# Optimization experiments

Hardware: AMD Instinct MI355X
Metric: run time of the kernel (lower is better)

The kernel has to match this reference:

```python
import jax, jax.numpy as jnp
import numpy as np

B, L, H = 16, 2048, 768
INNER = max(H // 2, 32)
RADIUS = 2
K_STEPS = 4
ETA = 0.1
ETA_DECAY = 0.9
MU_MAX = 10.0
LAM = 0.1


def _window_edges(length, radius):
    ei, ej = [], []
    for r in range(1, radius + 1):
        i = np.arange(length - r)
        ei.append(i)
        ej.append(i + r)
    return (jnp.asarray(np.concatenate(ei), jnp.int32),
            jnp.asarray(np.concatenate(ej), jnp.int32))


def setup_inputs() -> dict:
    key = jax.random.key(0)
    ks = jax.random.split(key, 6)
    hidden = jax.random.normal(ks[0], (B, L, H), jnp.float32)
    attention_mask = jnp.ones((B, L), jnp.int32)  # uniform full lengths -> single bucket, window path
    w1 = jax.random.normal(ks[1], (2, INNER), jnp.float32) * 0.2
    b1 = jnp.zeros((INNER,), jnp.float32)
    w2 = jax.random.normal(ks[2], (INNER, 1), jnp.float32) * 0.05
    b2 = jnp.zeros((1,), jnp.float32)
    wq = jax.random.normal(ks[3], (H, H), jnp.float32) * (1.0 / np.sqrt(H))
    bq = jnp.zeros((H,), jnp.float32)
    gamma = jnp.ones((H,), jnp.float32)
    beta = jnp.zeros((H,), jnp.float32)
    edges_i, edges_j = _window_edges(L, RADIUS)
    return dict(hidden=hidden, attention_mask=attention_mask, w1=w1, b1=b1,
                w2=w2, b2=b2, wq=wq, bq=bq, gamma=gamma, beta=beta,
                edges_i=edges_i, edges_j=edges_j)


def _friction(hidden, w1, b1, w2, b2, wq, bq, gamma, beta, edges_i, edges_j):
    eps = 1e-6
    q = hidden @ wq + bq                      # [B,L,H]
    state = hidden
    mu = None
    for step in range(K_STEPS):
        # edge weights from current state (recompute_mu=True)
        h_i = state[:, edges_i]               # [B,E,H] gather
        h_j = state[:, edges_j]
        diff = h_i - h_j
        dist = jnp.sqrt(jnp.sum(diff * diff, -1))
        n_i = jnp.maximum(jnp.sqrt(jnp.sum(h_i * h_i, -1)), eps)
        n_j = jnp.maximum(jnp.sqrt(jnp.sum(h_j * h_j, -1)), eps)
        cos = jnp.sum(h_i * h_j, -1) / (n_i * n_j)
        feats = jnp.stack([dist, cos], -1)    # [B,E,2]
        mid = jax.nn.gelu(feats @ w1 + b1, approximate=False)
        mu = jnp.minimum(jax.nn.softplus((mid @ w2 + b2)[..., 0]) + 1e-5, MU_MAX)  # [B,E]
        # normalized weighted graph Laplacian applied to state
        w = mu[..., None] * diff
        deg = jnp.zeros((state.shape[0], state.shape[1]), state.dtype)
        deg = deg.at[:, edges_i].add(mu).at[:, edges_j].add(mu)
        inv = jnp.maximum(deg, 1e-6) ** -0.5
        w = w * (inv[:, edges_i] * inv[:, edges_j])[..., None]
        lap = jnp.zeros_like(state).at[:, edges_i].add(w).at[:, edges_j].add(-w)
        state = state - (ETA * ETA_DECAY ** step) * (lap - q)
        # 1D chain smoothing with replicated boundaries
        left = jnp.concatenate([state[:, :1], state[:, :-1]], 1)
        right = jnp.concatenate([state[:, 1:], state[:, -1:]], 1)
        state = state - LAM * (2 * state - left - right)
    # edge energy with last mu and final state: 0.5 * sum_e mu_e ||s_i - s_j||^2
    df = state[:, edges_i] - state[:, edges_j]
    energy = 0.5 * jnp.sum(mu * jnp.sum(df * df, -1), axis=1)  # [B]
    res = state + hidden
    mean = jnp.mean(res, -1, keepdims=True)
    var = jnp.mean((res - mean) ** 2, -1, keepdims=True)
    out = (res - mean) / jnp.sqrt(var + 1e-5) * gamma + beta
    return out, energy


def reference(hidden, attention_mask, w1, b1, w2, b2, wq, bq, gamma, beta, edges_i, edges_j):
    # all masks are full-length ones -> single bucket, batched window path
    return _friction(hidden, w1, b1, w2, b2, wq, bq, gamma, beta, edges_i, edges_j)
```

## Files before the change

### kernel.cpp

```cpp
#include <hip/hip_runtime.h>
#include <hip/hip_bf16.h>
#include <math.h>

#define B_ 16
#define L_ 2048
#define H_ 768
#define INNER_ 384
#define MU_MAX_ 10.0f
#define LAM_ 0.1f
#define EDGES_ (2 * L_ - 3)

typedef short v8bf __attribute__((ext_vector_type(8)));
typedef float v4f  __attribute__((ext_vector_type(4)));

static __device__ __forceinline__ float wave_sum(float v) {
    #pragma unroll
    for (int o = 32; o > 0; o >>= 1) v += __shfl_xor(v, o, 64);
    return v;
}

static __device__ __forceinline__ float dot4(const float4& a, const float4& b) {
    return a.x * b.x + a.y * b.y + a.z * b.z + a.w * b.w;
}

static __device__ __forceinline__ void fma4(float4& a, float c, float4 x) {
    a.x = fmaf(c, x.x, a.x); a.y = fmaf(c, x.y, a.y);
    a.z = fmaf(c, x.z, a.z); a.w = fmaf(c, x.w, a.w);
}

static __device__ __forceinline__ ushort f2bf(float x) {
    unsigned u = __float_as_uint(x);
    u += 0x7fffu + ((u >> 16) & 1u);
    return (ushort)(u >> 16);
}

__global__ __launch_bounds__(256) void conv_wqt_kernel(
    const float* __restrict__ wq, ushort* __restrict__ wt)
{
    __shared__ float tile[64][65];
    int k0 = blockIdx.x * 64, n0 = blockIdx.y * 64;
    int t = threadIdx.x;
    #pragma unroll
    for (int it = 0; it < 16; ++it) {
        int lin = t + it * 256;
        int r = lin >> 6, c = lin & 63;
        tile[r][c] = wq[(size_t)(k0 + r) * H_ + n0 + c];
    }
    __syncthreads();
    #pragma unroll
    for (int it = 0; it < 16; ++it) {
        int lin = t + it * 256;
        int r = lin >> 6, c = lin & 63;
        wt[(size_t)(n0 + r) * H_ + k0 + c] = f2bf(tile[c][r]);
    }
}

#define GBM 128
#define GBN 128
#define GBK 64
#define LSTR 72

__global__ __launch_bounds__(256) void gemm_q_kernel(
    const float* __restrict__ A32, const ushort* __restrict__ Wt,
    const float* __restrict__ bias, float* __restrict__ C)
{
    __shared__ ushort As[GBM * LSTR];
    __shared__ ushort Bs[GBN * LSTR];
    const int K = H_, N = H_;
    int idx = blockIdx.x;
    int c = idx & 7, rest = idx >> 3;
    int n0 = (rest % 6) * GBN;
    int m0 = ((rest / 6) * 8 + c) * GBM;
    int t = threadIdx.x;
    int lane = t & 63, w = t >> 6;
    int wm = (w & 1) * 64, wn = (w >> 1) * 64;
    int row16 = lane & 15, quad = lane >> 4;

    v4f acc[4][4];
    #pragma unroll
    for (int i = 0; i < 4; ++i)
        #pragma unroll
        for (int j = 0; j < 4; ++j)
            acc[i][j] = (v4f){0.f, 0.f, 0.f, 0.f};

    float4 pf0[4], pf1[4];
    v8bf pfB[4];
    #pragma unroll
    for (int it = 0; it < 4; ++it) {
        int lin = t + it * 256;
        int r = lin >> 3, s = lin & 7;
        const float* ap = A32 + (size_t)(m0 + r) * K + s * 8;
        pf0[it] = *(const float4*)ap;
        pf1[it] = *(const float4*)(ap + 4);
        pfB[it] = *(const v8bf*)(Wt + (size_t)(n0 + r) * K + s * 8);
    }

    for (int kt = 0; kt < 12; ++kt) {
        int k0 = kt * GBK;
        #pragma unroll
        for (int it = 0; it < 4; ++it) {
            int lin = t + it * 256;
            int r = lin >> 3, s = lin & 7;
            ushort tmp[8] = { f2bf(pf0[it].x), f2bf(pf0[it].y), f2bf(pf0[it].z), f2bf(pf0[it].w),
                              f2bf(pf1[it].x), f2bf(pf1[it].y), f2bf(pf1[it].z), f2bf(pf1[it].w) };
            *(v8bf*)&As[r * LSTR + s * 8] = *(v8bf*)tmp;
            *(v8bf*)&Bs[r * LSTR + s * 8] = pfB[it];
        }
        if (kt < 11) {
            int kn = k0 + GBK;
            #pragma unroll
            for (int it = 0; it < 4; ++it) {
                int lin = t + it * 256;
                int r = lin >> 3, s = lin & 7;
                const float* ap = A32 + (size_t)(m0 + r) * K + kn + s * 8;
                pf0[it] = *(const float4*)ap;
                pf1[it] = *(const float4*)(ap + 4);
                pfB[it] = *(const v8bf*)(Wt + (size_t)(n0 + r) * K + kn + s * 8);
            }
        }
        __syncthreads();
        #pragma unroll
        for (int h = 0; h < 2; ++h) {
            v8bf af[4], bfv[4];
            #pragma unroll
            for (int i = 0; i < 4; ++i)
                af[i] = *(v8bf*)&As[(wm + i * 16 + row16) * LSTR + h * 32 + quad * 8];
            #pragma unroll
            for (int j = 0; j < 4; ++j)
                bfv[j] = *(v8bf*)&Bs[(wn + j * 16 + row16) * LSTR + h * 32 + quad * 8];
            #pragma unroll
            for (int i = 0; i < 4; ++i)
                #pragma unroll
                for (int j = 0; j < 4; ++j)
                    acc[i][j] = __builtin_amdgcn_mfma_f32_16x16x32_bf16(
                        af[i], bfv[j], acc[i][j], 0, 0, 0);
        }
        __syncthreads();
    }
    #pragma unroll
    for (int j = 0; j < 4; ++j) {
        int ncol = n0 + wn + j * 16 + row16;
        float bqv = bias[ncol];
        #pragma unroll
        for (int i = 0; i < 4; ++i) {
            int mrow = m0 + wm + i * 16 + quad * 4;
            #pragma unroll
            for (int r = 0; r < 4; ++r)
                C[(size_t)(mrow + r) * N + ncol] = acc[i][j][r] + bqv;
        }
    }
}

__global__ __launch_bounds__(256) void mu_pair_kernel(
    const float* __restrict__ src,
    const float* __restrict__ w1, const float* __restrict__ b1,
    const float* __restrict__ w2, const float* __restrict__ b2,
    float* __restrict__ mu)
{
    int blk = blockIdx.x;
    int chunk = (blk & 7) * ((B_ * L_ / 8) / 8) + (blk >> 3);
    int b = chunk >> 8;
    int p0 = (chunk & 255) * 8;
    int w = threadIdx.x >> 6, lane = threadIdx.x & 63;
    int t0 = p0 + 2 * w;

    const float* sB = src + (size_t)b * L_ * H_;
    int r2 = min(t0 + 2, L_ - 1), r3 = min(t0 + 3, L_ - 1);
    const float4* x0p = (const float4*)(sB + (size_t)t0 * H_);
    const float4* x1p = (const float4*)(sB + (size_t)(t0 + 1) * H_);
    const float4* x2p = (const float4*)(sB + (size_t)r2 * H_);
    const float4* x3p = (const float4*)(sB + (size_t)r3 * H_);

    float ss0 = 0.f, ss1 = 0.f, ss2 = 0.f, ss3 = 0.f;
    float d1a = 0.f, d1b = 0.f, d2a = 0.f, d2b = 0.f;
    #pragma unroll
    for (int ch = 0; ch < 3; ++ch) {
        int off = ch * 64 + lane;
        float4 x0 = x0p[off], x1 = x1p[off], x2 = x2p[off], x3 = x3p[off];
        ss0 += dot4(x0, x0); ss1 += dot4(x1, x1);
        ss2 += dot4(x2, x2); ss3 += dot4(x3, x3);
        d1a += dot4(x0, x1); d1b += dot4(x1, x2);
        d2a += dot4(x0, x2); d2b += dot4(x1, x3);
    }
    ss0 = wave_sum(ss0); ss1 = wave_sum(ss1); ss2 = wave_sum(ss2); ss3 = wave_sum(ss3);
    d1a = wave_sum(d1a); d1b = wave_sum(d1b); d2a = wave_sum(d2a); d2b = wave_sum(d2b);

    float dist[4], cosv[4];
    {
        float si[4] = {ss0, ss0, ss1, ss1};
        float sj[4] = {ss1, ss2, ss2, ss3};
        float dd[4] = {d1a, d2a, d1b, d2b};
        #pragma unroll
        for (int e = 0; e < 4; ++e) {
            dist[e] = sqrtf(fmaxf(si[e] + sj[e] - 2.f * dd[e], 0.f));
            cosv[e] = dd[e] / (fmaxf(sqrtf(si[e]), 1e-6f) * fmaxf(sqrtf(sj[e]), 1e-6f));
        }
    }
    float acc[4] = {0.f, 0.f, 0.f, 0.f};
    #pragma unroll
    for (int k = 0; k < 6; ++k) {
        int u = k * 64 + lane;
        float wd = w1[u], wc = w1[INNER_ + u], bb = b1[u], wv = w2[u];
        #pragma unroll
        for (int e = 0; e < 4; ++e) {
            float z = fmaf(dist[e], wd, fmaf(cosv[e], wc, bb));
            float g = 0.5f * z * (1.f + erff(z * 0.70710678118654752f));
            acc[e] = fmaf(g, wv, acc[e]);
        }
    }
    #pragma unroll
    for (int e = 0; e < 4; ++e) acc[e] = wave_sum(acc[e]);

    float b2v = b2[0];
    float muv[4];
    #pragma unroll
    for (int e = 0; e < 4; ++e) {
        float a = acc[e] + b2v;
        float sp = fmaxf(a, 0.f) + log1pf(expf(-fabsf(a)));
        muv[e] = fminf(sp + 1e-5f, MU_MAX_);
    }
    if (lane == 0) {
        float* mB = mu + (size_t)b * EDGES_;
        mB[t0] = muv[0];
        if (t0 < L_ - 2) {
            mB[(L_ - 1) + t0] = muv[1];
            mB[t0 + 1] = muv[2];
            if (t0 + 1 < L_ - 2) mB[(L_ - 1) + t0 + 1] = muv[3];
        }
    }
}

template <int LN>
__global__ __launch_bounds__(256) void upd_quad_kernel(
    const float* __restrict__ src, const float* __restrict__ q,
    const float* __restrict__ mu, float* __restrict__ dst,
    const float* __restrict__ hidden, const float* __restrict__ gamma,
    const float* __restrict__ beta, float* __restrict__ lnout, float coef)
{
    int blk = blockIdx.x;
    int chunk = (blk & 7) * ((B_ * L_ / 16) / 8) + (blk >> 3);
    int b = chunk >> 7;
    int p0 = (chunk & 127) * 16;
    int w = threadIdx.x >> 6, lane = threadIdx.x & 63;
    int t0 = p0 + 4 * w;

    const float* mp = mu + (size_t)b * EDGES_;
    float M1[11], M2[12];
    #pragma unroll
    for (int j = 0; j < 11; ++j) {
        int u = t0 - 4 + j;
        M1[j] = (u >= 0 && u < L_ - 1) ? mp[u] : 0.f;
    }
    #pragma unroll
    for (int j = 0; j < 12; ++j) {
        int u = t0 - 5 + j;
        M2[j] = (u >= 0 && u < L_ - 2) ? mp[(L_ - 1) + u] : 0.f;
    }
    float IV[10];
    #pragma unroll
    for (int d = 0; d < 10; ++d) {
        int u = t0 - 3 + d;
        if (u < 0 || u >= L_) { IV[d] = 0.f; }
        else {
            float deg = M1[d + 1] + M1[d] + M2[d + 2] + M2[d];
            IV[d] = 1.f / sqrtf(fmaxf(deg, 1e-6f));
        }
    }
    float C[4][7], e[4][3];
    #pragma unroll
    for (int r = 0; r < 4; ++r) {
        int p = t0 + r;
        float gwv[3];
        gwv[0] = (p == 0) ? 0.f : LAM_;
        gwv[2] = (p == L_ - 1) ? 0.f : LAM_;
        gwv[1] = 1.f - 2.f * LAM_ + ((p == 0 || p == L_ - 1) ? LAM_ : 0.f);
        #pragma unroll
        for (int d = 0; d < 7; ++d) C[r][d] = 0.f;
        #pragma unroll
        for (int i = 0; i < 3; ++i) {
            int j = r + i;
            float g = gwv[i];
            float wm2 = M2[j + 2] * IV[j + 2] * IV[j];
            float wm1 = M1[j + 2] * IV[j + 2] * IV[j + 1];
            float wp1 = M1[j + 3] * IV[j + 2] * IV[j + 3];
            float wp2 = M2[j + 4] * IV[j + 2] * IV[j + 4];
            float wsum = wm2 + wm1 + wp1 + wp2;
            C[r][i]     = fmaf(g * coef, wm2, C[r][i]);
            C[r][i + 1] = fmaf(g * coef, wm1, C[r][i + 1]);
            C[r][i + 2] = fmaf(g, fmaf(-coef, wsum, 1.f), C[r][i + 2]);
            C[r][i + 3] = fmaf(g * coef, wp1, C[r][i + 3]);
            C[r][i + 4] = fmaf(g * coef, wp2, C[r][i + 4]);
            e[r][i] = g * coef;
        }
    }

    const float* sB = src + (size_t)b * L_ * H_;
    const float* qB = q + (size_t)b * L_ * H_;
    const float* sp[10];
    #pragma unroll
    for (int u = 0; u < 10; ++u)
        sp[u] = sB + (size_t)min(max(t0 - 3 + u, 0), L_ - 1) * H_;
    const float* qp[6];
    #pragma unroll
    for (int u = 0; u < 6; ++u)
        qp[u] = qB + (size_t)min(max(t0 - 1 + u, 0), L_ - 1) * H_;

    float* dA = dst + ((size_t)b * L_ + t0) * H_;
    float4 res[4][3];
    #pragma unroll
    for (int ch = 0; ch < 3; ++ch) {
        int off = ch * 64 + lane;
        float4 S[10], Q[6];
        #pragma unroll
        for (int u = 0; u < 10; ++u) S[u] = ((const float4*)sp[u])[off];
        #pragma unroll
        for (int u = 0; u < 6; ++u) Q[u] = ((const float4*)qp[u])[off];
        #pragma unroll
        for (int r = 0; r < 4; ++r) {
            float4 a = {0.f, 0.f, 0.f, 0.f};
            #pragma unroll
            for (int d = 0; d < 7; ++d) fma4(a, C[r][d], S[r + d]);
            #pragma unroll
            for (int i = 0; i < 3; ++i) fma4(a, e[r][i], Q[r + i]);
            ((float4*)(dA + (size_t)r * H_))[off] = a;
            if (LN) res[r][ch] = a;
        }
    }

    if (LN) {
        const float* hB = hidden + ((size_t)b * L_ + t0) * H_;
        float* oB = lnout + ((size_t)b * L_ + t0) * H_;
        float sum[4], sq[4];
        #pragma unroll
        for (int r = 0; r < 4; ++r) {
            sum[r] = 0.f; sq[r] = 0.f;
            #pragma unroll
            for (int ch = 0; ch < 3; ++ch) {
                int off = ch * 64 + lane;
                float4 h = ((const float4*)(hB + (size_t)r * H_))[off];
                float4 x = res[r][ch];
                x.x += h.x; x.y += h.y; x.z += h.z; x.w += h.w;
                res[r][ch] = x;
                sum[r] += x.x + x.y + x.z + x.w;
                sq[r]  += x.x * x.x + x.y * x.y + x.z * x.z + x.w * x.w;
            }
        }
        #pragma unroll
        for (int r = 0; r < 4; ++r) { sum[r] = wave_sum(sum[r]); sq[r] = wave_sum(sq[r]); }
        #pragma unroll
        for (int r = 0; r < 4; ++r) {
            float mean = sum[r] * (1.f / H_);
            float var  = sq[r] * (1.f / H_) - mean * mean;
            float rs = 1.f / sqrtf(var + 1e-5f);
            #pragma unroll
            for (int ch = 0; ch < 3; ++ch) {
                int off = ch * 64 + lane;
                float4 g4 = ((const float4*)gamma)[off];
                float4 b4 = ((const float4*)beta)[off];
                float4 x = res[r][ch];
                float4 o;
                o.x = (x.x - mean) * rs * g4.x + b4.x;
                o.y = (x.y - mean) * rs * g4.y + b4.y;
                o.z = (x.z - mean) * rs * g4.z + b4.z;
                o.w = (x.w - mean) * rs * g4.w + b4.w;
                ((float4*)(oB + (size_t)r * H_))[off] = o;
            }
        }
    }
}

__global__ void zero_energy_kernel(float* __restrict__ e) {
    if (threadIdx.x < B_) e[threadIdx.x] = 0.f;
}

#define EPW 16
__global__ __launch_bounds__(256) void energy_kernel(
    const float* __restrict__ state, const int* __restrict__ ei, const int* __restrict__ ej,
    const float* __restrict__ mu, float* __restrict__ energy, int E)
{
    __shared__ float red[4];
    int wib = threadIdx.x >> 6;
    int lane = threadIdx.x & 63;
    int nchunk = (E + 63) / 64;
    int b = blockIdx.x / nchunk;
    int chunk = blockIdx.x - b * nchunk;
    int e0 = chunk * 64 + wib * EPW;
    const float* base = state + (size_t)b * L_ * H_;
    const float* muB = mu + (size_t)b * E;
    float part = 0.f;
    for (int k = 0; k < EPW; ++k) {
        int e = e0 + k;
        if (e >= E) break;
        int i = ei[e], j = ej[e];
        const float4* ri = (const float4*)(base + (size_t)i * H_);
        const float4* rj = (const float4*)(base + (size_t)j * H_);
        float s = 0.f;
        #pragma unroll
        for (int it = 0; it < 3; ++it) {
            float4 xi = ri[it * 64 + lane], xj = rj[it * 64 + lane];
            float dx = xi.x - xj.x, dy = xi.y - xj.y, dz = xi.z - xj.z, dw = xi.w - xj.w;
            s += dx*dx + dy*dy + dz*dz + dw*dw;
        }
        s = wave_sum(s);
        part += muB[e] * s;
    }
    if (lane == 0) red[wib] = part;
    __syncthreads();
    if (threadIdx.x == 0)
        atomicAdd(energy + b, 0.5f * (red[0] + red[1] + red[2] + red[3]));
}

extern "C" void kernel_launch(void* const* d_in, const int* in_sizes, int n_in,
                              void* d_out, int out_size, void* d_ws, size_t ws_size,
                              hipStream_t stream)
{
    const float* hidden = (const float*)d_in[0];
    const float* w1 = (const float*)d_in[2];
    const float* b1 = (const float*)d_in[3];
    const float* w2 = (const float*)d_in[4];
    const float* b2 = (const float*)d_in[5];
    const float* wq = (const float*)d_in[6];
    const float* bq = (const float*)d_in[7];
    const float* gamma = (const float*)d_in[8];
    const float* beta  = (const float*)d_in[9];
    const int* ei = (const int*)d_in[10];
    const int* ej = (const int*)d_in[11];
    int E = in_sizes[10];

    const size_t BLH = (size_t)B_ * L_ * H_;
    float* out = (float*)d_out;
    float* energy = out + BLH;

    float* q    = (float*)d_ws;
    float* bufA = q + BLH;
    float* bufB = bufA + BLH;
    float* mu   = bufB + BLH;
    ushort* wt  = (ushort*)(mu + (size_t)B_ * EDGES_);

    conv_wqt_kernel<<<dim3(H_ / 64, H_ / 64), 256, 0, stream>>>(wq, wt);
    gemm_q_kernel<<<(B_ * L_ / GBM) * (H_ / GBN), 256, 0, stream>>>(hidden, wt, bq, q);
    zero_energy_kernel<<<1, 64, 0, stream>>>(energy);

    const int NBP = B_ * L_ / 8;
    const int NBQ = B_ * L_ / 16;
    float coef = 0.1f;

    mu_pair_kernel<<<NBP, 256, 0, stream>>>(hidden, w1, b1, w2, b2, mu);
    upd_quad_kernel<0><<<NBQ, 256, 0, stream>>>(hidden, q, mu, bufA,
        hidden, gamma, beta, nullptr, coef);
    coef *= 0.9f;
    mu_pair_kernel<<<NBP, 256, 0, stream>>>(bufA, w1, b1, w2, b2, mu);
    upd_quad_kernel<0><<<NBQ, 256, 0, stream>>>(bufA, q, mu, bufB,
        hidden, gamma, beta, nullptr, coef);
    coef *= 0.9f;
    mu_pair_kernel<<<NBP, 256, 0, stream>>>(bufB, w1, b1, w2, b2, mu);
    upd_quad_kernel<0><<<NBQ, 256, 0, stream>>>(bufB, q, mu, bufA,
        hidden, gamma, beta, nullptr, coef);
    coef *= 0.9f;
    mu_pair_kernel<<<NBP, 256, 0, stream>>>(bufA, w1, b1, w2, b2, mu);
    upd_quad_kernel<1><<<NBQ, 256, 0, stream>>>(bufA, q, mu, bufB,
        hidden, gamma, beta, out, coef);

    int nchunk = (E + 63) / 64;
    energy_kernel<<<B_ * nchunk, 256, 0, stream>>>(bufB, ei, ej, mu, energy, E);
}
```

Baseline: 778.3 us.

## Fuse edge dot-product statistics into update kernel and split mu MLP

```diff
diff --git a/kernel.cpp b/kernel.cpp
--- a/kernel.cpp
+++ b/kernel.cpp
@@ -70,7 +70,7 @@
     int idx = blockIdx.x;
     int c = idx & 7, rest = idx >> 3;
     int n0 = (rest % 6) * GBN;
-    int m0 = ((rest / 6) * 8 + c) * GBM;
+    int m0 = (c * 32 + rest / 6) * GBM;
     int t = threadIdx.x;
     int lane = t & 63, w = t >> 6;
     int wm = (w & 1) * 64, wn = (w >> 1) * 64;
@@ -151,6 +151,25 @@
     }
 }
 
+static __device__ __forceinline__ float mu_mlp2(
+    float si, float sj, float dotij,
+    const float* w1d, const float* w1c, const float* b1v, const float* w2v,
+    float b2v)
+{
+    float dist = sqrtf(fmaxf(si + sj - 2.f * dotij, 0.f));
+    float cosv = dotij / (fmaxf(sqrtf(si), 1e-6f) * fmaxf(sqrtf(sj), 1e-6f));
+    float acc = 0.f;
+    #pragma unroll
+    for (int k = 0; k < 6; ++k) {
+        float z = fmaf(dist, w1d[k], fmaf(cosv, w1c[k], b1v[k]));
+        float g = 0.5f * z * (1.f + erff(z * 0.70710678118654752f));
+        acc = fmaf(g, w2v[k], acc);
+    }
+    acc = wave_sum(acc) + b2v;
+    float sp = fmaxf(acc, 0.f) + log1pf(expf(-fabsf(acc)));
+    return fminf(sp + 1e-5f, MU_MAX_);
+}
+
 __global__ __launch_bounds__(256) void mu_pair_kernel(
     const float* __restrict__ src,
     const float* __restrict__ w1, const float* __restrict__ b1,
@@ -230,10 +249,73 @@
     }
 }
 
-template <int LN>
+__global__ __launch_bounds__(256) void boundary_dots_kernel(
+    const float* __restrict__ src, float* __restrict__ d1S, float* __restrict__ d2S)
+{
+    int blk = blockIdx.x;
+    int chunk = (blk & 7) * 256 + (blk >> 3);
+    int g = chunk * 4 + (threadIdx.x >> 6);
+    int lane = threadIdx.x & 63;
+    int b = g >> 9;
+    int t0 = (g & 511) * 4;
+    const float* sB = src + (size_t)b * L_ * H_;
+    const float4* p2 = (const float4*)(sB + (size_t)min(t0 + 2, L_ - 1) * H_);
+    const float4* p3 = (const float4*)(sB + (size_t)min(t0 + 3, L_ - 1) * H_);
+    const float4* p4 = (const float4*)(sB + (size_t)min(t0 + 4, L_ - 1) * H_);
+    const float4* p5 = (const float4*)(sB + (size_t)min(t0 + 5, L_ - 1) * H_);
+    float a = 0.f, bb = 0.f, cc = 0.f;
+    #pragma unroll
+    for (int ch = 0; ch < 3; ++ch) {
+        int off = ch * 64 + lane;
+        float4 x2 = p2[off], x3 = p3[off], x4 = p4[off], x5 = p5[off];
+        a  += dot4(x3, x4);
+        bb += dot4(x2, x4);
+        cc += dot4(x3, x5);
+    }
+    a = wave_sum(a); bb = wave_sum(bb); cc = wave_sum(cc);
+    if (lane == 0) {
+        size_t base = (size_t)b * L_;
+        d1S[base + t0 + 3] = a;
+        d2S[base + t0 + 2] = bb;
+        d2S[base + t0 + 3] = cc;
+    }
+}
+
+__global__ __launch_bounds__(256) void mu_mlp_kernel(
+    const float* __restrict__ ssS, const float* __restrict__ d1S,
+    const float* __restrict__ d2S,
+    const float* __restrict__ w1, const float* __restrict__ b1,
+    const float* __restrict__ w2, const float* __restrict__ b2,
+    float* __restrict__ mu)
+{
+    int rg = blockIdx.x * 4 + (threadIdx.x >> 6);
+    int lane = threadIdx.x & 63;
+    int b = rg >> 11;
+    int t = rg & (L_ - 1);
+    if (t >= L_ - 1) return;
+    size_t base = (size_t)b * L_;
+    float ss0 = ssS[base + t], ss1 = ssS[base + t + 1], d1 = d1S[base + t];
+    float w1d[6], w1c[6], b1v[6], w2v[6];
+    #pragma unroll
+    for (int k = 0; k < 6; ++k) {
+        int u = k * 64 + lane;
+        w1d[k] = w1[u]; w1c[k] = w1[INNER_ + u]; b1v[k] = b1[u]; w2v[k] = w2[u];
+    }
+    float b2v = b2[0];
+    float m1 = mu_mlp2(ss0, ss1, d1, w1d, w1c, b1v, w2v, b2v);
+    if (lane == 0) mu[(size_t)b * EDGES_ + t] = m1;
+    if (t < L_ - 2) {
+        float ss2 = ssS[base + t + 2], d2 = d2S[base + t];
+        float m2v = mu_mlp2(ss0, ss2, d2, w1d, w1c, b1v, w2v, b2v);
+        if (lane == 0) mu[(size_t)b * EDGES_ + (L_ - 1) + t] = m2v;
+    }
+}
+
+template <int LN, int EMIT>
 __global__ __launch_bounds__(256) void upd_quad_kernel(
     const float* __restrict__ src, const float* __restrict__ q,
     const float* __restrict__ mu, float* __restrict__ dst,
+    float* __restrict__ ssS, float* __restrict__ d1S, float* __restrict__ d2S,
     const float* __restrict__ hidden, const float* __restrict__ gamma,
     const float* __restrict__ beta, float* __restrict__ lnout, float coef)
 {
@@ -307,6 +389,9 @@
 
     float* dA = dst + ((size_t)b * L_ + t0) * H_;
     float4 res[4][3];
+    float ssp[4] = {0.f, 0.f, 0.f, 0.f};
+    float d1p[3] = {0.f, 0.f, 0.f};
+    float d2p[2] = {0.f, 0.f};
     #pragma unroll
     for (int ch = 0; ch < 3; ++ch) {
         int off = ch * 64 + lane;
@@ -315,6 +400,7 @@
         for (int u = 0; u < 10; ++u) S[u] = ((const float4*)sp[u])[off];
         #pragma unroll
         for (int u = 0; u < 6; ++u) Q[u] = ((const float4*)qp[u])[off];
+        float4 a4[4];
         #pragma unroll
         for (int r = 0; r < 4; ++r) {
             float4 a = {0.f, 0.f, 0.f, 0.f};
@@ -323,7 +409,34 @@
             #pragma unroll
             for (int i = 0; i < 3; ++i) fma4(a, e[r][i], Q[r + i]);
             ((float4*)(dA + (size_t)r * H_))[off] = a;
+            a4[r] = a;
             if (LN) res[r][ch] = a;
+        }
+        if (EMIT) {
+            #pragma unroll
+            for (int r = 0; r < 4; ++r) ssp[r] += dot4(a4[r], a4[r]);
+            #pragma unroll
+            for (int r = 0; r < 3; ++r) d1p[r] += dot4(a4[r], a4[r + 1]);
+            #pragma unroll
+            for (int r = 0; r < 2; ++r) d2p[r] += dot4(a4[r], a4[r + 2]);
+        }
+    }
+
+    if (EMIT) {
+        #pragma unroll
+        for (int r = 0; r < 4; ++r) ssp[r] = wave_sum(ssp[r]);
+        #pragma unroll
+        for (int r = 0; r < 3; ++r) d1p[r] = wave_sum(d1p[r]);
+        #pragma unroll
+        for (int r = 0; r < 2; ++r) d2p[r] = wave_sum(d2p[r]);
+        if (lane == 0) {
+            size_t base = (size_t)b * L_;
+            #pragma unroll
+            for (int r = 0; r < 4; ++r) ssS[base + t0 + r] = ssp[r];
+            #pragma unroll
+            for (int r = 0; r < 3; ++r) d1S[base + t0 + r] = d1p[r];
+            #pragma unroll
+            for (int r = 0; r < 2; ++r) d2S[base + t0 + r] = d2p[r];
         }
     }
 
@@ -436,6 +549,9 @@
     float* bufB = bufA + BLH;
     float* mu   = bufB + BLH;
     ushort* wt  = (ushort*)(mu + (size_t)B_ * EDGES_);
+    float* ssS  = (float*)(wt + (size_t)H_ * H_);
+    float* d1S  = ssS + (size_t)B_ * L_;
+    float* d2S  = d1S + (size_t)B_ * L_;
 
     conv_wqt_kernel<<<dim3(H_ / 64, H_ / 64), 256, 0, stream>>>(wq, wt);
     gemm_q_kernel<<<(B_ * L_ / GBM) * (H_ / GBN), 256, 0, stream>>>(hidden, wt, bq, q);
@@ -443,23 +559,28 @@
 
     const int NBP = B_ * L_ / 8;
     const int NBQ = B_ * L_ / 16;
+    const int NBB = B_ * L_ / 16;
+    const int NBM = B_ * L_ / 4;
     float coef = 0.1f;
 
     mu_pair_kernel<<<NBP, 256, 0, stream>>>(hidden, w1, b1, w2, b2, mu);
-    upd_quad_kernel<0><<<NBQ, 256, 0, stream>>>(hidden, q, mu, bufA,
-        hidden, gamma, beta, nullptr, coef);
+    upd_quad_kernel<0, 1><<<NBQ, 256, 0, stream>>>(hidden, q, mu, bufA,
+        ssS, d1S, d2S, hidden, gamma, beta, nullptr, coef);
     coef *= 0.9f;
-    mu_pair_kernel<<<NBP, 256, 0, stream>>>(bufA, w1, b1, w2, b2, mu);
-    upd_quad_kernel<0><<<NBQ, 256, 0, stream>>>(bufA, q, mu, bufB,
-        hidden, gamma, beta, nullptr, coef);
+    boundary_dots_kernel<<<NBB, 256, 0, stream>>>(bufA, d1S, d2S);
+    mu_mlp_kernel<<<NBM, 256, 0, stream>>>(ssS, d1S, d2S, w1, b1, w2, b2, mu);
+    upd_quad_kernel<0, 1><<<NBQ, 256, 0, stream>>>(bufA, q, mu, bufB,
+        ssS, d1S, d2S, hidden, gamma, beta, nullptr, coef);
     coef *= 0.9f;
-    mu_pair_kernel<<<NBP, 256, 0, stream>>>(bufB, w1, b1, w2, b2, mu);
-    upd_quad_kernel<0><<<NBQ, 256, 0, stream>>>(bufB, q, mu, bufA,
-        hidden, gamma, beta, nullptr, coef);
+    boundary_dots_kernel<<<NBB, 256, 0, stream>>>(bufB, d1S, d2S);
+    mu_mlp_kernel<<<NBM, 256, 0, stream>>>(ssS, d1S, d2S, w1, b1, w2, b2, mu);
+    upd_quad_kernel<0, 1><<<NBQ, 256, 0, stream>>>(bufB, q, mu, bufA,
+        ssS, d1S, d2S, hidden, gamma, beta, nullptr, coef);
     coef *= 0.9f;
-    mu_pair_kernel<<<NBP, 256, 0, stream>>>(bufA, w1, b1, w2, b2, mu);
-    upd_quad_kernel<1><<<NBQ, 256, 0, stream>>>(bufA, q, mu, bufB,
-        hidden, gamma, beta, out, coef);
+    boundary_dots_kernel<<<NBB, 256, 0, stream>>>(bufA, d1S, d2S);
+    mu_mlp_kernel<<<NBM, 256, 0, stream>>>(ssS, d1S, d2S, w1, b1, w2, b2, mu);
+    upd_quad_kernel<1, 0><<<NBQ, 256, 0, stream>>>(bufA, q, mu, bufB,
+        ssS, d1S, d2S, hidden, gamma, beta, out, coef);
 
     int nchunk = (E + 63) / 64;
     energy_kernel<<<B_ * nchunk, 256, 0, stream>>>(bufB, ei, ej, mu, energy, E);
```

Result: no change. 785.3 us (+0.9%).
